# Kernel tuning notes

Measured on AMD Instinct MI355X. Metric: run time of the kernel, lower is better.

## Reference

```python
import jax, jax.numpy as jnp
import numpy as np

D_HIDDEN = 1024
N_HEADS = 16
D_HEAD = 64
B, N = 4, 1024
EPS = 1e-5


def _lin(x, w, b):
    # torch Linear: y = x @ W^T + b, w: [out, in]
    return jnp.einsum('...i,oi->...o', x, w) + b


def _ln(x, g, b):
    m = jnp.mean(x, axis=-1, keepdims=True)
    v = jnp.mean(jnp.square(x - m), axis=-1, keepdims=True)
    return (x - m) * jax.lax.rsqrt(v + EPS) * g + b


def setup_inputs() -> dict:
    key = jax.random.key(0)
    ks = jax.random.split(key, 20)
    d = D_HIDDEN
    s = 0.02
    inp = {
        'x': jax.random.normal(ks[0], (B, N, d), jnp.float32),
        'time_emb': jax.random.normal(ks[1], (B, d), jnp.float32),
        'ln1_g': jnp.ones((d,), jnp.float32),
        'ln1_b': jnp.zeros((d,), jnp.float32),
        's1_w': jax.random.normal(ks[2], (d, d), jnp.float32) * s,
        's1_b': jnp.zeros((d,), jnp.float32),
        'o1_w': jax.random.normal(ks[3], (d, d), jnp.float32) * s,
        'o1_b': jnp.zeros((d,), jnp.float32),
        'qkv_w': jax.random.normal(ks[4], (3 * d, d), jnp.float32) * s,
        'qkv_b': jnp.zeros((3 * d,), jnp.float32),
        'proj_w': jax.random.normal(ks[5], (d, d), jnp.float32) * s,
        'proj_b': jnp.zeros((d,), jnp.float32),
        'ln2_g': jnp.ones((d,), jnp.float32),
        'ln2_b': jnp.zeros((d,), jnp.float32),
        's2_w': jax.random.normal(ks[6], (d, d), jnp.float32) * s,
        's2_b': jnp.zeros((d,), jnp.float32),
        'o2_w': jax.random.normal(ks[7], (d, d), jnp.float32) * s,
        'o2_b': jnp.zeros((d,), jnp.float32),
        'up_w': jax.random.normal(ks[8], (4 * d, d), jnp.float32) * s,
        'up_b': jnp.zeros((4 * d,), jnp.float32),
        'down_w': jax.random.normal(ks[9], (d, 4 * d), jnp.float32) * s,
        'down_b': jnp.zeros((d,), jnp.float32),
    }
    return inp


def reference(x, time_emb, ln1_g, ln1_b, s1_w, s1_b, o1_w, o1_b,
              qkv_w, qkv_b, proj_w, proj_b, ln2_g, ln2_b,
              s2_w, s2_b, o2_w, o2_b, up_w, up_b, down_w, down_b):
    d = D_HIDDEN

    def ada(h, sw, sb, ow, ob):
        scale = _lin(time_emb, sw, sb)[:, None, :]   # [B,1,d]
        offset = _lin(time_emb, ow, ob)[:, None, :]
        return (1.0 + scale) * h + offset

    # attention branch
    h = ada(_ln(x, ln1_g, ln1_b), s1_w, s1_b, o1_w, o1_b)
    qkv = _lin(h, qkv_w, qkv_b)                       # [B,N,3d]
    q, k, v = jnp.split(qkv, 3, axis=-1)
    q = q.reshape(B, N, N_HEADS, D_HEAD)
    k = k.reshape(B, N, N_HEADS, D_HEAD)
    v = v.reshape(B, N, N_HEADS, D_HEAD)
    wei = jnp.einsum('bnhd,bmhd->bhnm', q, k) * (D_HEAD ** -0.5)
    wei = jax.nn.softmax(wei, axis=-1)
    attn = jnp.einsum('bhnm,bmhd->bnhd', wei, v).reshape(B, N, d)
    x = x + _lin(attn, proj_w, proj_b)

    # mlp branch (torch nn.GELU default = exact erf gelu)
    h = ada(_ln(x, ln2_g, ln2_b), s2_w, s2_b, o2_w, o2_b)
    h = jax.nn.gelu(_lin(h, up_w, up_b), approximate=False)
    x = x + _lin(h, down_w, down_b)
    return x, time_emb
```

## Files before the change

### kernel.cpp

```cpp
#include <hip/hip_runtime.h>
#include <hip/hip_bf16.h>
#include <math.h>

#define DH 1024
#define BB 4
#define NN 1024
#define NH 16
#define HD 64

typedef __attribute__((ext_vector_type(8))) short bf16x8;
typedef __attribute__((ext_vector_type(4))) float f32x4;
typedef __attribute__((ext_vector_type(4))) unsigned int u32x4;
typedef unsigned short u16;
typedef unsigned int u32;

static __device__ __forceinline__ u16 f2bf(float f) {
  __hip_bfloat16 h = __float2bfloat16(f);
  return *reinterpret_cast<u16*>(&h);
}
static __device__ __forceinline__ float bf2f(u16 x) {
  return __uint_as_float((unsigned)x << 16);
}

#define MFMA16(a, b, c) __builtin_amdgcn_mfma_f32_16x16x32_bf16(a, b, c, 0, 0, 0)
#define VMCNT(n) asm volatile("s_waitcnt vmcnt(" #n ")" ::: "memory")
#define MEMFENCE asm volatile("" ::: "memory")
#define BAR() do { __builtin_amdgcn_s_barrier(); MEMFENCE; } while (0)

static __device__ __forceinline__ void async16(const void* g, void* l) {
  __builtin_amdgcn_global_load_lds(
      (const __attribute__((address_space(1))) void*)g,
      (__attribute__((address_space(3))) void*)l, 16, 0, 0);
}

__global__ void cvt_all_kernel(const float* __restrict__ wq, const float* __restrict__ wp,
                               const float* __restrict__ wu, const float* __restrict__ wd,
                               u16* __restrict__ oq, u16* __restrict__ op,
                               u16* __restrict__ ou, u16* __restrict__ od) {
  int i = blockIdx.x * 256 + threadIdx.x;
  const float* src; u16* dst; int off;
  if (i < 786432)            { src = wq; dst = oq; off = i; }
  else if (i < 1048576)      { src = wp; dst = op; off = i - 786432; }
  else if (i < 2097152)      { src = wu; dst = ou; off = i - 1048576; }
  else                       { src = wd; dst = od; off = i - 2097152; }
  float4 v = reinterpret_cast<const float4*>(src)[off];
  ushort4 o;
  o.x = f2bf(v.x); o.y = f2bf(v.y); o.z = f2bf(v.z); o.w = f2bf(v.w);
  reinterpret_cast<ushort4*>(dst)[off] = o;
}

__global__ __launch_bounds__(256) void adaln_kernel(
    const float* __restrict__ e,
    const float* __restrict__ w_s1, const float* __restrict__ b_s1,
    const float* __restrict__ w_o1, const float* __restrict__ b_o1,
    const float* __restrict__ w_s2, const float* __restrict__ b_s2,
    const float* __restrict__ w_o2, const float* __restrict__ b_o2,
    float* __restrict__ out) {
  int tid = threadIdx.x, wid = tid >> 6, lane = tid & 63;
  int mat = blockIdx.y;
  const float* w; const float* bs; float addc;
  if (mat == 0)      { w = w_s1; bs = b_s1; addc = 1.f; }
  else if (mat == 1) { w = w_o1; bs = b_o1; addc = 0.f; }
  else if (mat == 2) { w = w_s2; bs = b_s2; addc = 1.f; }
  else               { w = w_o2; bs = b_o2; addc = 0.f; }
  int col = blockIdx.x * 4 + wid;
  float a0 = 0.f, a1 = 0.f, a2 = 0.f, a3 = 0.f;
  const float* wc_ = w + (size_t)col * DH;
  for (int i = 0; i < 16; ++i) {
    int k = i * 64 + lane;
    float wv = wc_[k];
    a0 += wv * e[k];
    a1 += wv * e[DH + k];
    a2 += wv * e[2 * DH + k];
    a3 += wv * e[3 * DH + k];
  }
  #pragma unroll
  for (int msk = 32; msk; msk >>= 1) {
    a0 += __shfl_xor(a0, msk); a1 += __shfl_xor(a1, msk);
    a2 += __shfl_xor(a2, msk); a3 += __shfl_xor(a3, msk);
  }
  if (lane == 0) {
    float bb = bs[col] + addc;
    out[mat * (4 * DH) + 0 * DH + col] = a0 + bb;
    out[mat * (4 * DH) + 1 * DH + col] = a1 + bb;
    out[mat * (4 * DH) + 2 * DH + col] = a2 + bb;
    out[mat * (4 * DH) + 3 * DH + col] = a3 + bb;
  }
}

__global__ __launch_bounds__(256) void ln_mod_kernel(
    const float* __restrict__ x, const float* __restrict__ g, const float* __restrict__ bta,
    const float* __restrict__ sp, const float* __restrict__ off, u16* __restrict__ out) {
  int row = blockIdx.x;
  int b = row >> 10;
  int tid = threadIdx.x;
  int wid = tid >> 6, lane = tid & 63;
  const float4 xv = reinterpret_cast<const float4*>(x + (size_t)row * DH)[tid];
  float s = xv.x + xv.y + xv.z + xv.w;
  float ss = xv.x * xv.x + xv.y * xv.y + xv.z * xv.z + xv.w * xv.w;
  #pragma unroll
  for (int m = 32; m; m >>= 1) { s += __shfl_xor(s, m); ss += __shfl_xor(ss, m); }
  __shared__ float red[8];
  if (lane == 0) { red[wid] = s; red[4 + wid] = ss; }
  __syncthreads();
  s = red[0] + red[1] + red[2] + red[3];
  ss = red[4] + red[5] + red[6] + red[7];
  float mean = s * (1.f / DH);
  float var = ss * (1.f / DH) - mean * mean;
  float rstd = rsqrtf(var + 1e-5f);
  int c = tid * 4;
  const float* spb = sp + b * DH + c;
  const float* offb = off + b * DH + c;
  float y0 = (xv.x - mean) * rstd * g[c + 0] + bta[c + 0];
  float y1 = (xv.y - mean) * rstd * g[c + 1] + bta[c + 1];
  float y2 = (xv.z - mean) * rstd * g[c + 2] + bta[c + 2];
  float y3 = (xv.w - mean) * rstd * g[c + 3] + bta[c + 3];
  ushort4 o;
  o.x = f2bf(spb[0] * y0 + offb[0]);
  o.y = f2bf(spb[1] * y1 + offb[1]);
  o.z = f2bf(spb[2] * y2 + offb[2]);
  o.w = f2bf(spb[3] * y3 + offb[3]);
  reinterpret_cast<ushort4*>(out + (size_t)row * DH)[tid] = o;
}

enum { EPI_BF16 = 0, EPI_GELU = 1, EPI_PART = 2 };

template <int EPI>
__global__ __launch_bounds__(512, 2) void gemmT_kernel(
    const u16* __restrict__ A, const u16* __restrict__ W,
    const float* __restrict__ bias, void* __restrict__ outp,
    int N, int K, int KTunused) {
  extern __shared__ u16 lds[];
  u16* Ab = lds;
  u16* Bb = lds + 24576;
  int tid = threadIdx.x;
  int wid = tid >> 6, lane = tid & 63;
  int l15 = lane & 15, l4 = lane >> 4;
  int wr = wid >> 2, wc = wid & 3;

  int nwg = gridDim.x * gridDim.y;
  int lin = blockIdx.y * gridDim.x + blockIdx.x;
  int q8 = nwg >> 3;
  int lin2 = (lin & 7) * q8 + (lin >> 3);
  int bx = lin2 % gridDim.x, by = lin2 / gridDim.x;
  int m0 = by * 256, n0 = bx * 128;
  int k0 = blockIdx.z * 1024;

  f32x4 acc[8][2] = {};

  const u16* Abase = A + (size_t)m0 * K + k0;
  const u16* Wbase = W + (size_t)n0 * K + k0;
  int i0 = tid, i1 = 512 + tid;
  int r0 = i0 >> 2, c0 = (i0 & 3) ^ ((r0 >> 1) & 3);
  int r1 = i1 >> 2, c1 = (i1 & 3) ^ ((r1 >> 1) & 3);
  int rB = tid >> 2, cB = (tid & 3) ^ ((rB >> 1) & 3);
  size_t gA0 = (size_t)r0 * K + c0 * 8;
  size_t gA1 = (size_t)r1 * K + c1 * 8;
  size_t gB0 = (size_t)rB * K + cB * 8;
  int lbA0 = (wid * 64) * 8;
  int lbA1 = (512 + wid * 64) * 8;

  auto stage = [&](int tt, int bi) {
    int qa = bi * 8192, qb = bi * 4096;
    const u16* Ak = Abase + tt * 32;
    const u16* Wk = Wbase + tt * 32;
    async16(Ak + gA0, &Ab[qa + lbA0]);
    async16(Ak + gA1, &Ab[qa + lbA1]);
    async16(Wk + gB0, &Bb[qb + lbA0]);
  };

  auto compute = [&](int bi) {
    int qa = bi * 8192, qb = bi * 4096;
    bf16x8 af[8], bfr[2];
    #pragma unroll
    for (int m = 0; m < 8; ++m) {
      int row = wr * 128 + m * 16 + l15;
      int ps = l4 ^ ((row >> 1) & 3);
      af[m] = *reinterpret_cast<const bf16x8*>(&Ab[qa + row * 32 + ps * 8]);
    }
    #pragma unroll
    for (int n = 0; n < 2; ++n) {
      int row = wc * 32 + n * 16 + l15;
      int ps = l4 ^ ((row >> 1) & 3);
      bfr[n] = *reinterpret_cast<const bf16x8*>(&Bb[qb + row * 32 + ps * 8]);
    }
    #pragma unroll
    for (int m = 0; m < 8; ++m)
      #pragma unroll
      for (int n = 0; n < 2; ++n)
        acc[m][n] = MFMA16(af[m], bfr[n], acc[m][n]);
  };

  stage(0, 0);
  stage(1, 1);
  for (int tb = 0; tb < 30; tb += 3) {
    VMCNT(3); BAR(); stage(tb + 2, 2); compute(0);
    VMCNT(3); BAR(); stage(tb + 3, 0); compute(1);
    VMCNT(3); BAR(); stage(tb + 4, 1); compute(2);
  }
  VMCNT(3); BAR(); compute(0);
  VMCNT(0); BAR(); compute(1);

  int M = gridDim.y * 256;
  u16* pout = (u16*)outp + (size_t)blockIdx.z * M * N;
  #pragma unroll
  for (int n = 0; n < 2; ++n) {
    int col = n0 + wc * 32 + n * 16 + l15;
    float bv = (EPI == EPI_PART) ? 0.f : bias[col];
    #pragma unroll
    for (int m = 0; m < 8; ++m) {
      #pragma unroll
      for (int r = 0; r < 4; ++r) {
        int rowg = m0 + wr * 128 + m * 16 + l4 * 4 + r;
        float v = acc[m][n][r] + bv;
        if (EPI == EPI_GELU) {
          v = 0.5f * v * (1.f + erff(v * 0.70710678118f));
          ((u16*)outp)[(size_t)rowg * N + col] = f2bf(v);
        } else if (EPI == EPI_BF16) {
          ((u16*)outp)[(size_t)rowg * N + col] = f2bf(v);
        } else {
          pout[(size_t)rowg * N + col] = f2bf(v);
        }
      }
    }
  }
}

enum { OEPI_BF16 = 0, OEPI_GELU = 1, OEPI_RES = 2 };

template <int EPI>
__global__ __launch_bounds__(256, 3) void gemm_bt_kernel(
    const u16* __restrict__ A, const u16* __restrict__ W,
    const float* __restrict__ bias, const float* __restrict__ resid,
    void* __restrict__ outp, int N, int K) {
  __shared__ __align__(16) u16 As[2][128 * 32];
  __shared__ __align__(16) u16 Ws[2][128 * 32];
  int tid = threadIdx.x;
  int wid = tid >> 6, lane = tid & 63;
  int l15 = lane & 15, l4 = lane >> 4;
  int m0 = blockIdx.y * 128, n0 = blockIdx.x * 128;
  int wr = wid >> 1, wc = wid & 1;
  f32x4 acc[4][4] = {};

  const int KT = K >> 5;
  int idx0 = tid, idx1 = 256 + tid;
  int rowA0 = idx0 >> 2, gs0 = (idx0 & 3) ^ ((rowA0 >> 1) & 3);
  int rowA1 = idx1 >> 2, gs1 = (idx1 & 3) ^ ((rowA1 >> 1) & 3);
  const u16* Abase = A + (size_t)m0 * K;
  const u16* Wbase = W + (size_t)n0 * K;
  int lb0 = (wid * 64) * 8;
  int lb1 = (256 + wid * 64) * 8;

  auto stage = [&](int buf, int kt) {
    const u16* Ak = Abase + kt * 32;
    const u16* Wk = Wbase + kt * 32;
    async16(Ak + (size_t)rowA0 * K + gs0 * 8, &As[buf][lb0]);
    async16(Wk + (size_t)rowA0 * K + gs0 * 8, &Ws[buf][lb0]);
    async16(Ak + (size_t)rowA1 * K + gs1 * 8, &As[buf][lb1]);
    async16(Wk + (size_t)rowA1 * K + gs1 * 8, &Ws[buf][lb1]);
  };

  auto compute = [&](int buf) {
    bf16x8 af[4], wf[4];
    #pragma unroll
    for (int m = 0; m < 4; ++m) {
      int row = wr * 64 + m * 16 + l15;
      int ps = l4 ^ ((row >> 1) & 3);
      af[m] = *reinterpret_cast<const bf16x8*>(&As[buf][row * 32 + ps * 8]);
    }
    #pragma unroll
    for (int n = 0; n < 4; ++n) {
      int row = wc * 64 + n * 16 + l15;
      int ps = l4 ^ ((row >> 1) & 3);
      wf[n] = *reinterpret_cast<const bf16x8*>(&Ws[buf][row * 32 + ps * 8]);
    }
    #pragma unroll
    for (int m = 0; m < 4; ++m)
      #pragma unroll
      for (int n = 0; n < 4; ++n)
        acc[m][n] = MFMA16(af[m], wf[n], acc[m][n]);
  };

  stage(0, 0);
  __syncthreads();
  int buf = 0;
  for (int kt = 0; kt < KT - 1; ++kt) {
    stage(buf ^ 1, kt + 1);
    compute(buf);
    __syncthreads();
    buf ^= 1;
  }
  compute(buf);

  #pragma unroll
  for (int n = 0; n < 4; ++n) {
    int col = n0 + wc * 64 + n * 16 + l15;
    float bv = bias[col];
    #pragma unroll
    for (int m = 0; m < 4; ++m) {
      #pragma unroll
      for (int r = 0; r < 4; ++r) {
        int rowg = m0 + wr * 64 + m * 16 + l4 * 4 + r;
        float v = acc[m][n][r] + bv;
        if (EPI == OEPI_GELU) {
          v = 0.5f * v * (1.f + erff(v * 0.70710678118f));
          ((u16*)outp)[(size_t)rowg * N + col] = f2bf(v);
        } else if (EPI == OEPI_BF16) {
          ((u16*)outp)[(size_t)rowg * N + col] = f2bf(v);
        } else {
          ((float*)outp)[(size_t)rowg * N + col] = v + resid[(size_t)rowg * N + col];
        }
      }
    }
  }
}

__global__ __launch_bounds__(256) void reduce4_kernel(
    const u16* __restrict__ part, const float* __restrict__ x2,
    const float* __restrict__ bias, const float* __restrict__ te,
    float* __restrict__ out) {
  size_t i = (size_t)blockIdx.x * 256 + threadIdx.x;
  const size_t MN = (size_t)4096 * 1024;
  float4 xr = reinterpret_cast<const float4*>(x2)[i];
  int col = (int)((i * 4) & 1023);
  float4 bv = *reinterpret_cast<const float4*>(&bias[col]);
  float a0 = xr.x + bv.x, a1 = xr.y + bv.y, a2 = xr.z + bv.z, a3 = xr.w + bv.w;
  #pragma unroll
  for (int p = 0; p < 4; ++p) {
    ushort4 u = reinterpret_cast<const ushort4*>(part + p * MN)[i];
    a0 += bf2f(u.x); a1 += bf2f(u.y); a2 += bf2f(u.z); a3 += bf2f(u.w);
  }
  float4 o; o.x = a0; o.y = a1; o.z = a2; o.w = a3;
  reinterpret_cast<float4*>(out)[i] = o;
  if (blockIdx.x < 16) {
    int ii = blockIdx.x * 256 + threadIdx.x;
    out[4096 * 1024 + ii] = te[ii];
  }
}

__global__ __launch_bounds__(256) void vt_kernel(const u16* __restrict__ qkvb,
                                                 u16* __restrict__ vT) {
  __shared__ u16 L[64 * 66];
  int bh = blockIdx.y;
  int b = bh >> 4, h = bh & 15;
  int nt = blockIdx.x;
  int t = threadIdx.x;
  const u16* src = qkvb + ((size_t)b * 1024 + nt * 64) * 3072 + 2048 + h * 64;
  int j = t >> 3, s = t & 7;
  bf16x8 r0 = *reinterpret_cast<const bf16x8*>(src + (size_t)j * 3072 + s * 8);
  bf16x8 r1 = *reinterpret_cast<const bf16x8*>(src + (size_t)(j + 32) * 3072 + s * 8);
  #pragma unroll
  for (int e = 0; e < 8; ++e) {
    L[(s * 8 + e) * 66 + j] = r0[e];
    L[(s * 8 + e) * 66 + j + 32] = r1[e];
  }
  __syncthreads();
  int d = t & 63, cp = t >> 6;
  u16* dst = vT + ((size_t)bh * 64 + d) * 1024 + nt * 64;
  #pragma unroll
  for (int half = 0; half < 2; ++half) {
    int cs = cp + half * 4;
    bf16x8 o;
    #pragma unroll
    for (int c = 0; c < 8; ++c) o[c] = L[d * 66 + cs * 8 + c];
    *reinterpret_cast<bf16x8*>(dst + cs * 8) = o;
  }
}

__global__ __launch_bounds__(256, 4) void attn_kernel(
    const u16* __restrict__ qkv, const u16* __restrict__ vT, u16* __restrict__ out) {
  __shared__ __align__(16) u16 Ks[2][4096];
  __shared__ __align__(16) u16 Vs[2][4096];
  int tid = threadIdx.x, wid = tid >> 6, lane = tid & 63;
  int l15 = lane & 15, l4 = lane >> 4;
  int L = blockIdx.y * gridDim.x + blockIdx.x;
  int qt = (L >> 3) & 15;
  int bh = (L & 7) | ((L >> 7) << 3);
  int b = bh >> 4, h = bh & 15;
  const size_t SN = 3 * DH;
  const u16* qb = qkv + (size_t)b * NN * SN + h * HD;
  const u16* kb = qb + DH;
  const u16* vtb = vT + (size_t)bh * 64 * 1024;

  int qrow = qt * 64 + wid * 16 + l15;
  bf16x8 qf[2];
  #pragma unroll
  for (int ks = 0; ks < 2; ++ks)
    qf[ks] = *reinterpret_cast<const bf16x8*>(qb + (size_t)qrow * SN + ks * 32 + l4 * 8);

  float m_ = -1e30f, l_ = 0.f;
  f32x4 o_[4] = {};

  int laA = ((l4 * 2) & 3) * 16 + l15;
  int laB = ((l4 * 2 + 1) & 3) * 16 + l15;
  bool nbhi = (l4 >> 1) != 0;

  int iA = tid, iB = 256 + tid;
  int jA = iA >> 3, sA = iA & 7, gsA = sA ^ (jA & 7);
  int jB = iB >> 3, sB = iB & 7, gsB = sB ^ (jB & 7);

  auto stageKV = [&](int bufn, int t) {
    const u16* kt = kb + (size_t)t * 64 * SN;
    async16(kt + (size_t)jA * SN + gsA * 8, &Ks[bufn][iA * 8]);
    async16(kt + (size_t)jB * SN + gsB * 8, &Ks[bufn][iB * 8]);
    const u16* vt = vtb + (size_t)t * 64;
    async16(vt + (size_t)jA * 1024 + gsA * 8, &Vs[bufn][iA * 8]);
    async16(vt + (size_t)jB * 1024 + gsB * 8, &Vs[bufn][iB * 8]);
  };

  stageKV(0, 0);
  __syncthreads();

  int buf = 0;
  for (int t = 0; t < 16; ++t) {
    if (t < 15) stageKV(buf ^ 1, t + 1);

    f32x4 sa[4];
    #pragma unroll
    for (int nb = 0; nb < 4; ++nb) {
      f32x4 s = {};
      #pragma unroll
      for (int ks = 0; ks < 2; ++ks) {
        int j = nb * 16 + l15;
        int ps = (ks * 4 + l4) ^ (j & 7);
        bf16x8 kf = *reinterpret_cast<const bf16x8*>(&Ks[buf][j * 64 + ps * 8]);
        s = MFMA16(kf, qf[ks], s);
      }
      sa[nb] = s * 0.125f;
    }

    float pm = sa[0][0];
    #pragma unroll
    for (int nb = 0; nb < 4; ++nb)
      #pragma unroll
      for (int r = 0; r < 4; ++r)
        if (nb || r) pm = fmaxf(pm, sa[nb][r]);
    pm = fmaxf(pm, __shfl_xor(pm, 16));
    pm = fmaxf(pm, __shfl_xor(pm, 32));

    if (!__all(pm - m_ <= 8.f)) {
      float mn = fmaxf(m_, pm);
      float corr = __expf(m_ - mn);
      m_ = mn;
      l_ *= corr;
      float c0 = __shfl(corr, l4 * 4 + 0);
      float c1 = __shfl(corr, l4 * 4 + 1);
      float c2 = __shfl(corr, l4 * 4 + 2);
      float c3 = __shfl(corr, l4 * 4 + 3);
      #pragma unroll
      for (int nd = 0; nd < 4; ++nd) {
        o_[nd][0] *= c0; o_[nd][1] *= c1; o_[nd][2] *= c2; o_[nd][3] *= c3;
      }
    }

    float ts = 0.f;
    u32 pk[4][2];
    #pragma unroll
    for (int nb = 0; nb < 4; ++nb) {
      float p0 = __expf(sa[nb][0] - m_);
      float p1 = __expf(sa[nb][1] - m_);
      float p2 = __expf(sa[nb][2] - m_);
      float p3 = __expf(sa[nb][3] - m_);
      ts += (p0 + p1) + (p2 + p3);
      pk[nb][0] = (u32)f2bf(p0) | ((u32)f2bf(p1) << 16);
      pk[nb][1] = (u32)f2bf(p2) | ((u32)f2bf(p3) << 16);
    }
    ts += __shfl_xor(ts, 16);
    ts += __shfl_xor(ts, 32);
    l_ += ts;

    __builtin_amdgcn_s_setprio(1);
    #pragma unroll
    for (int ks = 0; ks < 2; ++ks) {
      int nlo = ks * 2, nhi = ks * 2 + 1;
      u32 a00 = __shfl((int)pk[nlo][0], laA), a01 = __shfl((int)pk[nlo][1], laA);
      u32 a10 = __shfl((int)pk[nhi][0], laA), a11 = __shfl((int)pk[nhi][1], laA);
      u32 b00 = __shfl((int)pk[nlo][0], laB), b01 = __shfl((int)pk[nlo][1], laB);
      u32 b10 = __shfl((int)pk[nhi][0], laB), b11 = __shfl((int)pk[nhi][1], laB);
      u32x4 wv;
      wv[0] = nbhi ? a10 : a00;
      wv[1] = nbhi ? a11 : a01;
      wv[2] = nbhi ? b10 : b00;
      wv[3] = nbhi ? b11 : b01;
      bf16x8 pa = __builtin_bit_cast(bf16x8, wv);
      #pragma unroll
      for (int nd = 0; nd < 4; ++nd) {
        int d = nd * 16 + l15;
        int psv = (ks * 4 + l4) ^ (d & 7);
        bf16x8 vf = *reinterpret_cast<const bf16x8*>(&Vs[buf][d * 64 + psv * 8]);
        o_[nd] = MFMA16(pa, vf, o_[nd]);
      }
    }
    __builtin_amdgcn_s_setprio(0);

    if (t < 15) __syncthreads();
    buf ^= 1;
  }

  float li0 = __shfl(l_, l4 * 4 + 0);
  float li1 = __shfl(l_, l4 * 4 + 1);
  float li2 = __shfl(l_, l4 * 4 + 2);
  float li3 = __shfl(l_, l4 * 4 + 3);
  float inv[4] = { 1.f / li0, 1.f / li1, 1.f / li2, 1.f / li3 };
  u16* ob = out + (size_t)b * NN * DH + h * HD;
  #pragma unroll
  for (int nd = 0; nd < 4; ++nd) {
    #pragma unroll
    for (int r = 0; r < 4; ++r) {
      int q = qt * 64 + wid * 16 + l4 * 4 + r;
      ob[(size_t)q * DH + nd * 16 + l15] = f2bf(o_[nd][r] * inv[r]);
    }
  }
}

extern "C" void kernel_launch(void* const* d_in, const int* in_sizes, int n_in,
                              void* d_out, int out_size, void* d_ws, size_t ws_size,
                              hipStream_t stream) {
  (void)in_sizes; (void)n_in; (void)out_size; (void)ws_size;
  const float* x      = (const float*)d_in[0];
  const float* te     = (const float*)d_in[1];
  const float* ln1_g  = (const float*)d_in[2];
  const float* ln1_b  = (const float*)d_in[3];
  const float* s1_w   = (const float*)d_in[4];
  const float* s1_b   = (const float*)d_in[5];
  const float* o1_w   = (const float*)d_in[6];
  const float* o1_b   = (const float*)d_in[7];
  const float* qkv_w  = (const float*)d_in[8];
  const float* qkv_b  = (const float*)d_in[9];
  const float* proj_w = (const float*)d_in[10];
  const float* proj_b = (const float*)d_in[11];
  const float* ln2_g  = (const float*)d_in[12];
  const float* ln2_b  = (const float*)d_in[13];
  const float* s2_w   = (const float*)d_in[14];
  const float* s2_b   = (const float*)d_in[15];
  const float* o2_w   = (const float*)d_in[16];
  const float* o2_b   = (const float*)d_in[17];
  const float* up_w   = (const float*)d_in[18];
  const float* up_b   = (const float*)d_in[19];
  const float* down_w = (const float*)d_in[20];
  const float* down_b = (const float*)d_in[21];

  char* ws = (char*)d_ws;
  size_t off = 0;
  auto alloc = [&](size_t bytes) { void* p = ws + off; off += (bytes + 255) & ~255ull; return p; };
  u16*   wq   = (u16*)  alloc((size_t)3072 * 1024 * 2);
  u16*   wp   = (u16*)  alloc((size_t)1024 * 1024 * 2);
  u16*   wu   = (u16*)  alloc((size_t)4096 * 1024 * 2);
  u16*   h1   = (u16*)  alloc((size_t)4096 * 1024 * 2);
  u16*   qkvb = (u16*)  alloc((size_t)4096 * 3072 * 2);
  u16*   att  = (u16*)  alloc((size_t)4096 * 1024 * 2);
  u16*   h2   = (u16*)  alloc((size_t)4096 * 1024 * 2);
  u16*   wd   = (u16*)  alloc((size_t)1024 * 4096 * 2);
  float* x2   = (float*)alloc((size_t)4096 * 1024 * 4);
  u16*   upb  = (u16*)  alloc((size_t)4096 * 4096 * 2);
  float* ada  = (float*)alloc((size_t)4 * 4 * 1024 * 4);
  float* sp1 = ada, *off1 = ada + 4096, *sp2 = ada + 8192, *off2 = ada + 12288;
  u16*   part = wq;
  u16*   vT   = h1;

  cvt_all_kernel<<<12288, 256, 0, stream>>>(qkv_w, proj_w, up_w, down_w, wq, wp, wu, wd);
  adaln_kernel<<<dim3(256, 4), 256, 0, stream>>>(te, s1_w, s1_b, o1_w, o1_b, s2_w, s2_b, o2_w, o2_b, ada);
  ln_mod_kernel<<<4096, 256, 0, stream>>>(x, ln1_g, ln1_b, sp1, off1, h1);
  gemmT_kernel<EPI_BF16><<<dim3(24, 16, 1), 512, 73728, stream>>>(h1, wq, qkv_b, qkvb, 3072, 1024, 32);
  vt_kernel<<<dim3(16, 64), 256, 0, stream>>>(qkvb, vT);
  attn_kernel<<<dim3(16, 64), 256, 0, stream>>>(qkvb, vT, att);
  gemm_bt_kernel<OEPI_RES><<<dim3(8, 32), 256, 0, stream>>>(att, wp, proj_b, x, x2, 1024, 1024);
  ln_mod_kernel<<<4096, 256, 0, stream>>>(x2, ln2_g, ln2_b, sp2, off2, h2);
  gemmT_kernel<EPI_GELU><<<dim3(32, 16, 1), 512, 73728, stream>>>(h2, wu, up_b, upb, 4096, 1024, 32);
  gemmT_kernel<EPI_PART><<<dim3(8, 16, 4), 512, 73728, stream>>>(upb, wd, nullptr, part, 1024, 4096, 32);
  reduce4_kernel<<<4096, 256, 0, stream>>>(part, x2, down_b, te, (float*)d_out);
}
```

Measured before the change: 252.2 us.

## Reshape gemmT warp tiling to 4x4 and reuse it for projection GEMM

Changes the per-warp tile in the 256x128 triple-buffered GEMM from 128x32 (8x2 MFMAs) to 64x64 (4x4 MFMAs), cutting per-step LDS fragment loads from 10 to 8. It also drops the separate double-buffered 128x128 gemm_bt kernel and routes the attention output projection with residual add through gemmT via a new EPI_RES epilogue. The projection GEMM now launches 128 workgroups instead of 256, which may leave part of the GPU idle for that stage.

Result: no change. 253.7 us (+0.6%).

```diff
diff --git a/kernel.cpp b/kernel.cpp
--- a/kernel.cpp
+++ b/kernel.cpp
@@ -123,20 +123,20 @@
   reinterpret_cast<ushort4*>(out + (size_t)row * DH)[tid] = o;
 }
 
-enum { EPI_BF16 = 0, EPI_GELU = 1, EPI_PART = 2 };
+enum { EPI_BF16 = 0, EPI_GELU = 1, EPI_PART = 2, EPI_RES = 3 };
 
 template <int EPI>
 __global__ __launch_bounds__(512, 2) void gemmT_kernel(
     const u16* __restrict__ A, const u16* __restrict__ W,
-    const float* __restrict__ bias, void* __restrict__ outp,
-    int N, int K, int KTunused) {
+    const float* __restrict__ bias, const float* __restrict__ resid,
+    void* __restrict__ outp, int N, int K) {
   extern __shared__ u16 lds[];
   u16* Ab = lds;
   u16* Bb = lds + 24576;
   int tid = threadIdx.x;
   int wid = tid >> 6, lane = tid & 63;
   int l15 = lane & 15, l4 = lane >> 4;
-  int wr = wid >> 2, wc = wid & 3;
+  int wr = wid >> 1, wc = wid & 1;
 
   int nwg = gridDim.x * gridDim.y;
   int lin = blockIdx.y * gridDim.x + blockIdx.x;
@@ -146,7 +146,7 @@
   int m0 = by * 256, n0 = bx * 128;
   int k0 = blockIdx.z * 1024;
 
-  f32x4 acc[8][2] = {};
+  f32x4 acc[4][4] = {};
 
   const u16* Abase = A + (size_t)m0 * K + k0;
   const u16* Wbase = W + (size_t)n0 * K + k0;
@@ -171,23 +171,23 @@
 
   auto compute = [&](int bi) {
     int qa = bi * 8192, qb = bi * 4096;
-    bf16x8 af[8], bfr[2];
-    #pragma unroll
-    for (int m = 0; m < 8; ++m) {
-      int row = wr * 128 + m * 16 + l15;
+    bf16x8 af[4], bfr[4];
+    #pragma unroll
+    for (int m = 0; m < 4; ++m) {
+      int row = wr * 64 + m * 16 + l15;
       int ps = l4 ^ ((row >> 1) & 3);
       af[m] = *reinterpret_cast<const bf16x8*>(&Ab[qa + row * 32 + ps * 8]);
     }
     #pragma unroll
-    for (int n = 0; n < 2; ++n) {
-      int row = wc * 32 + n * 16 + l15;
+    for (int n = 0; n < 4; ++n) {
+      int row = wc * 64 + n * 16 + l15;
       int ps = l4 ^ ((row >> 1) & 3);
       bfr[n] = *reinterpret_cast<const bf16x8*>(&Bb[qb + row * 32 + ps * 8]);
     }
     #pragma unroll
-    for (int m = 0; m < 8; ++m)
-      #pragma unroll
-      for (int n = 0; n < 2; ++n)
+    for (int m = 0; m < 4; ++m)
+      #pragma unroll
+      for (int n = 0; n < 4; ++n)
         acc[m][n] = MFMA16(af[m], bfr[n], acc[m][n]);
   };
 
@@ -204,111 +204,24 @@
   int M = gridDim.y * 256;
   u16* pout = (u16*)outp + (size_t)blockIdx.z * M * N;
   #pragma unroll
-  for (int n = 0; n < 2; ++n) {
-    int col = n0 + wc * 32 + n * 16 + l15;
+  for (int n = 0; n < 4; ++n) {
+    int col = n0 + wc * 64 + n * 16 + l15;
     float bv = (EPI == EPI_PART) ? 0.f : bias[col];
     #pragma unroll
-    for (int m = 0; m < 8; ++m) {
+    for (int m = 0; m < 4; ++m) {
       #pragma unroll
       for (int r = 0; r < 4; ++r) {
-        int rowg = m0 + wr * 128 + m * 16 + l4 * 4 + r;
+        int rowg = m0 + wr * 64 + m * 16 + l4 * 4 + r;
         float v = acc[m][n][r] + bv;
         if (EPI == EPI_GELU) {
           v = 0.5f * v * (1.f + erff(v * 0.70710678118f));
           ((u16*)outp)[(size_t)rowg * N + col] = f2bf(v);
         } else if (EPI == EPI_BF16) {
           ((u16*)outp)[(size_t)rowg * N + col] = f2bf(v);
+        } else if (EPI == EPI_RES) {
+          ((float*)outp)[(size_t)rowg * N + col] = v + resid[(size_t)rowg * N + col];
         } else {
           pout[(size_t)rowg * N + col] = f2bf(v);
-        }
-      }
-    }
-  }
-}
-
-enum { OEPI_BF16 = 0, OEPI_GELU = 1, OEPI_RES = 2 };
-
-template <int EPI>
-__global__ __launch_bounds__(256, 3) void gemm_bt_kernel(
-    const u16* __restrict__ A, const u16* __restrict__ W,
-    const float* __restrict__ bias, const float* __restrict__ resid,
-    void* __restrict__ outp, int N, int K) {
-  __shared__ __align__(16) u16 As[2][128 * 32];
-  __shared__ __align__(16) u16 Ws[2][128 * 32];
-  int tid = threadIdx.x;
-  int wid = tid >> 6, lane = tid & 63;
-  int l15 = lane & 15, l4 = lane >> 4;
-  int m0 = blockIdx.y * 128, n0 = blockIdx.x * 128;
-  int wr = wid >> 1, wc = wid & 1;
-  f32x4 acc[4][4] = {};
-
-  const int KT = K >> 5;
-  int idx0 = tid, idx1 = 256 + tid;
-  int rowA0 = idx0 >> 2, gs0 = (idx0 & 3) ^ ((rowA0 >> 1) & 3);
-  int rowA1 = idx1 >> 2, gs1 = (idx1 & 3) ^ ((rowA1 >> 1) & 3);
-  const u16* Abase = A + (size_t)m0 * K;
-  const u16* Wbase = W + (size_t)n0 * K;
-  int lb0 = (wid * 64) * 8;
-  int lb1 = (256 + wid * 64) * 8;
-
-  auto stage = [&](int buf, int kt) {
-    const u16* Ak = Abase + kt * 32;
-    const u16* Wk = Wbase + kt * 32;
-    async16(Ak + (size_t)rowA0 * K + gs0 * 8, &As[buf][lb0]);
-    async16(Wk + (size_t)rowA0 * K + gs0 * 8, &Ws[buf][lb0]);
-    async16(Ak + (size_t)rowA1 * K + gs1 * 8, &As[buf][lb1]);
-    async16(Wk + (size_t)rowA1 * K + gs1 * 8, &Ws[buf][lb1]);
-  };
-
-  auto compute = [&](int buf) {
-    bf16x8 af[4], wf[4];
-    #pragma unroll
-    for (int m = 0; m < 4; ++m) {
-      int row = wr * 64 + m * 16 + l15;
-      int ps = l4 ^ ((row >> 1) & 3);
-      af[m] = *reinterpret_cast<const bf16x8*>(&As[buf][row * 32 + ps * 8]);
-    }
-    #pragma unroll
-    for (int n = 0; n < 4; ++n) {
-      int row = wc * 64 + n * 16 + l15;
-      int ps = l4 ^ ((row >> 1) & 3);
-      wf[n] = *reinterpret_cast<const bf16x8*>(&Ws[buf][row * 32 + ps * 8]);
-    }
-    #pragma unroll
-    for (int m = 0; m < 4; ++m)
-      #pragma unroll
-      for (int n = 0; n < 4; ++n)
-        acc[m][n] = MFMA16(af[m], wf[n], acc[m][n]);
-  };
-
-  stage(0, 0);
-  __syncthreads();
-  int buf = 0;
-  for (int kt = 0; kt < KT - 1; ++kt) {
-    stage(buf ^ 1, kt + 1);
-    compute(buf);
-    __syncthreads();
-    buf ^= 1;
-  }
-  compute(buf);
-
-  #pragma unroll
-  for (int n = 0; n < 4; ++n) {
-    int col = n0 + wc * 64 + n * 16 + l15;
-    float bv = bias[col];
-    #pragma unroll
-    for (int m = 0; m < 4; ++m) {
-      #pragma unroll
-      for (int r = 0; r < 4; ++r) {
-        int rowg = m0 + wr * 64 + m * 16 + l4 * 4 + r;
-        float v = acc[m][n][r] + bv;
-        if (EPI == OEPI_GELU) {
-          v = 0.5f * v * (1.f + erff(v * 0.70710678118f));
-          ((u16*)outp)[(size_t)rowg * N + col] = f2bf(v);
-        } else if (EPI == OEPI_BF16) {
-          ((u16*)outp)[(size_t)rowg * N + col] = f2bf(v);
-        } else {
-          ((float*)outp)[(size_t)rowg * N + col] = v + resid[(size_t)rowg * N + col];
         }
       }
     }
@@ -561,12 +474,12 @@
   cvt_all_kernel<<<12288, 256, 0, stream>>>(qkv_w, proj_w, up_w, down_w, wq, wp, wu, wd);
   adaln_kernel<<<dim3(256, 4), 256, 0, stream>>>(te, s1_w, s1_b, o1_w, o1_b, s2_w, s2_b, o2_w, o2_b, ada);
   ln_mod_kernel<<<4096, 256, 0, stream>>>(x, ln1_g, ln1_b, sp1, off1, h1);
-  gemmT_kernel<EPI_BF16><<<dim3(24, 16, 1), 512, 73728, stream>>>(h1, wq, qkv_b, qkvb, 3072, 1024, 32);
+  gemmT_kernel<EPI_BF16><<<dim3(24, 16, 1), 512, 73728, stream>>>(h1, wq, qkv_b, nullptr, qkvb, 3072, 1024);
   vt_kernel<<<dim3(16, 64), 256, 0, stream>>>(qkvb, vT);
   attn_kernel<<<dim3(16, 64), 256, 0, stream>>>(qkvb, vT, att);
-  gemm_bt_kernel<OEPI_RES><<<dim3(8, 32), 256, 0, stream>>>(att, wp, proj_b, x, x2, 1024, 1024);
+  gemmT_kernel<EPI_RES><<<dim3(8, 16, 1), 512, 73728, stream>>>(att, wp, proj_b, x, x2, 1024, 1024);
   ln_mod_kernel<<<4096, 256, 0, stream>>>(x2, ln2_g, ln2_b, sp2, off2, h2);
-  gemmT_kernel<EPI_GELU><<<dim3(32, 16, 1), 512, 73728, stream>>>(h2, wu, up_b, upb, 4096, 1024, 32);
-  gemmT_kernel<EPI_PART><<<dim3(8, 16, 4), 512, 73728, stream>>>(upb, wd, nullptr, part, 1024, 4096, 32);
+  gemmT_kernel<EPI_GELU><<<dim3(32, 16, 1), 512, 73728, stream>>>(h2, wu, up_b, nullptr, upb, 4096, 1024);
+  gemmT_kernel<EPI_PART><<<dim3(8, 16, 4), 512, 73728, stream>>>(upb, wd, nullptr, nullptr, part, 1024, 4096);
   reduce4_kernel<<<4096, 256, 0, stream>>>(part, x2, down_b, te, (float*)d_out);
 }
```
